# Performance work log

Hardware: AMD Instinct MI355X
Metric: run time of the kernel (lower is better)

Reference implementation:

```python
import jax, jax.numpy as jnp
import numpy as np
import math

B, S, DIM, H, KVH = 2, 2048, 2048, 16, 4
HD = DIM // H          # 128
G = H // KVH           # 4 (GQA repeat factor)
NEG = -1e9             # fp32 additive mask value (matches torch path)


def _rotate_half(x):
    x1, x2 = jnp.split(x, 2, axis=-1)
    return jnp.concatenate([-x2, x1], axis=-1)


def setup_inputs() -> dict:
    key = jax.random.key(0)
    ks = jax.random.split(key, 8)
    hidden_states = jax.random.normal(ks[0], (B, S, DIM), jnp.float32)
    # standard RoPE tables [S, HD]
    inv_freq = 1.0 / (10000.0 ** (jnp.arange(0, HD, 2, dtype=jnp.float32) / HD))
    freqs = jnp.outer(jnp.arange(S, dtype=jnp.float32), inv_freq)
    emb = jnp.concatenate([freqs, freqs], axis=-1)
    position_cos = jnp.cos(emb)
    position_sin = jnp.sin(emb)
    alibi_bias = jax.random.normal(ks[1], (B, S, S), jnp.float32) * 0.01
    attention_mask = jnp.zeros((B, 1, 1, S), jnp.float32)
    sc = 0.02
    wq = jax.random.normal(ks[2], (DIM, DIM), jnp.float32) * sc
    wk = jax.random.normal(ks[3], (DIM, KVH * HD), jnp.float32) * sc
    wv = jax.random.normal(ks[4], (DIM, KVH * HD), jnp.float32) * sc
    wo = jax.random.normal(ks[5], (DIM, DIM), jnp.float32) * sc
    return {"hidden_states": hidden_states, "position_cos": position_cos,
            "position_sin": position_sin, "alibi_bias": alibi_bias,
            "attention_mask": attention_mask, "wq": wq, "wk": wk, "wv": wv, "wo": wo}


def reference(hidden_states, position_cos, position_sin, alibi_bias,
              attention_mask, wq, wk, wv, wo):
    b, s, d = hidden_states.shape
    # projections (weights stored as [in, out])
    q = (hidden_states @ wq).reshape(b, s, H, HD).transpose(0, 2, 1, 3)      # [B,H,S,HD]
    k = (hidden_states @ wk).reshape(b, s, KVH, HD).transpose(0, 2, 1, 3)    # [B,KVH,S,HD]
    v = (hidden_states @ wv).reshape(b, s, KVH, HD).transpose(0, 2, 1, 3)
    # RoPE
    cos = position_cos[None, None]  # [1,1,S,HD]
    sin = position_sin[None, None]
    q = q * cos + _rotate_half(q) * sin
    k = k * cos + _rotate_half(k) * sin
    # GQA repeat kv heads
    k = jnp.repeat(k, G, axis=1)   # [B,H,S,HD]
    v = jnp.repeat(v, G, axis=1)
    scores = jnp.einsum('bhqd,bhkd->bhqk', q, k) * (1.0 / math.sqrt(HD))
    causal = jnp.triu(jnp.full((s, s), NEG, jnp.float32), 1)
    scores = scores + causal + alibi_bias[:, None, :, :] + attention_mask
    attn = jax.nn.softmax(scores.astype(jnp.float32), axis=-1).astype(q.dtype)
    out = jnp.einsum('bhqk,bhkd->bhqd', attn, v)                              # [B,H,S,HD]
    out = out.transpose(0, 2, 1, 3).reshape(b, s, d)
    return out @ wo
```

## Files before the change

kernel.cpp:

```cpp
#include <hip/hip_runtime.h>
#include <hip/hip_bf16.h>

#define Bb   2
#define Ss   2048
#define Dd   2048
#define Hh   16
#define KVHh 4
#define HDd  128
#define QKVW 3072

typedef __bf16 bf16x8 __attribute__((ext_vector_type(8)));
typedef float f32x4 __attribute__((ext_vector_type(4)));

__device__ __forceinline__ unsigned short f2bf(float f) {
    unsigned u = __float_as_uint(f);
    unsigned r = (u + 0x7FFFu + ((u >> 16) & 1u)) >> 16;
    return (unsigned short)r;
}
__device__ __forceinline__ float bfu2f(unsigned short u) {
    return __uint_as_float(((unsigned)u) << 16);
}

#define GLOAD16(g, l) __builtin_amdgcn_global_load_lds( \
    (const __attribute__((address_space(1))) unsigned int*)(g), \
    (__attribute__((address_space(3))) unsigned int*)(l), 16, 0, 0)

__global__ __launch_bounds__(256)
void cast_bf16(const float* __restrict__ X, unsigned short* __restrict__ Y)
{
    int idx = blockIdx.x * 256 + threadIdx.x;
    float4 v = reinterpret_cast<const float4*>(X)[idx];
    ushort4 o;
    o.x = f2bf(v.x); o.y = f2bf(v.y); o.z = f2bf(v.z); o.w = f2bf(v.w);
    reinterpret_cast<ushort4*>(Y)[idx] = o;
}

__global__ __launch_bounds__(256)
void wt_cast_all(const float* __restrict__ wq, const float* __restrict__ wk,
                 const float* __restrict__ wv, const float* __restrict__ wo,
                 unsigned short* __restrict__ wqkvT, unsigned short* __restrict__ woT)
{
    __shared__ float tile[32][33];
    int id = blockIdx.x;
    const float* W; unsigned short* WT; int N, kx, ny;
    if (id < 4096)      {            W = wq; WT = wqkvT;                        N = 2048; kx = id & 63; ny = id >> 6; }
    else if (id < 5120) { id -= 4096; W = wk; WT = wqkvT + (size_t)2048 * 2048; N = 512;  kx = id & 63; ny = id >> 6; }
    else if (id < 6144) { id -= 5120; W = wv; WT = wqkvT + (size_t)2560 * 2048; N = 512;  kx = id & 63; ny = id >> 6; }
    else                { id -= 6144; W = wo; WT = woT;                         N = 2048; kx = id & 63; ny = id >> 6; }
    const int K = 2048;
    int k0 = kx * 32, n0 = ny * 32;
    int tx = threadIdx.x & 31, ty = threadIdx.x >> 5;
    #pragma unroll
    for (int i = 0; i < 32; i += 8)
        tile[ty + i][tx] = W[(size_t)(k0 + ty + i) * N + n0 + tx];
    __syncthreads();
    #pragma unroll
    for (int i = 0; i < 32; i += 8)
        WT[(size_t)(n0 + ty + i) * K + k0 + tx] = f2bf(tile[tx][ty + i]);
}

template<bool BF16OUT>
__global__ __launch_bounds__(512, 2)
void gemm256(const unsigned short* __restrict__ A,
             const unsigned short* __restrict__ BT,
             void* __restrict__ Cv, int M, int N, int K)
{
    __shared__ __align__(16) unsigned short sA[4][256 * 32];
    __shared__ __align__(16) unsigned short sB[4][256 * 32];
    const int tid  = threadIdx.x;
    const int w    = tid >> 6;
    const int lane = tid & 63;
    const int m    = lane & 15;
    const int quad = lane >> 4;
    const int wm   = w >> 2;
    const int wn   = w & 3;
    const int m0   = blockIdx.y * 256, n0 = blockIdx.x * 256;

    const int srow = tid >> 2;
    const int scol = (tid & 3) ^ (((tid >> 5) & 1) << 1);
    const int chk  = quad ^ (((m >> 3) & 1) << 1);

    f32x4 acc[8][4];
    #pragma unroll
    for (int fm = 0; fm < 8; ++fm)
        #pragma unroll
        for (int fn = 0; fn < 4; ++fn) acc[fm][fn] = (f32x4){0.f, 0.f, 0.f, 0.f};

    auto STAGE2 = [&](int T, int h) {
        const int buf = T & 3;
        GLOAD16(A  + (size_t)(m0 + h * 128 + srow) * K + T * 32 + scol * 8,
                (char*)sA + buf * 16384 + h * 8192 + w * 1024);
        GLOAD16(BT + (size_t)(n0 + h * 128 + srow) * K + T * 32 + scol * 8,
                (char*)sB + buf * 16384 + h * 8192 + w * 1024);
    };

    const int NT = K >> 5;

    STAGE2(0, 0); STAGE2(0, 1); STAGE2(1, 0); STAGE2(1, 1);
    asm volatile("s_waitcnt vmcnt(4)" ::: "memory");
    __builtin_amdgcn_s_barrier();
    __builtin_amdgcn_sched_barrier(0);

    #pragma unroll 1
    for (int t = 0; t < NT; ++t) {
        const int buf = t & 3;
        const char* ab = (const char*)sA + buf * 16384 + wm * 8192;
        const char* bb = (const char*)sB + buf * 16384 + (wn >> 1) * 8192 + (wn & 1) * 4096;

        bf16x8 bf[4], af[4];
        #pragma unroll
        for (int fn = 0; fn < 4; ++fn)
            bf[fn] = *(const bf16x8*)(bb + (fn * 16 + m) * 64 + chk * 16);
        #pragma unroll
        for (int j = 0; j < 4; ++j)
            af[j] = *(const bf16x8*)(ab + (j * 16 + m) * 64 + chk * 16);
        if (t + 2 < NT) STAGE2(t + 2, 0);
        __builtin_amdgcn_sched_barrier(0);
        __builtin_amdgcn_s_barrier();
        __builtin_amdgcn_sched_barrier(0);
        __builtin_amdgcn_s_setprio(1);
        #pragma unroll
        for (int j = 0; j < 4; ++j)
            #pragma unroll
            for (int fn = 0; fn < 4; ++fn)
                acc[j][fn] = __builtin_amdgcn_mfma_f32_16x16x32_bf16(
                    af[j], bf[fn], acc[j][fn], 0, 0, 0);
        __builtin_amdgcn_s_setprio(0);
        __builtin_amdgcn_s_barrier();
        __builtin_amdgcn_sched_barrier(0);

        #pragma unroll
        for (int j = 0; j < 4; ++j)
            af[j] = *(const bf16x8*)(ab + ((4 + j) * 16 + m) * 64 + chk * 16);
        if (t + 2 < NT) STAGE2(t + 2, 1);
        __builtin_amdgcn_sched_barrier(0);
        __builtin_amdgcn_s_barrier();
        __builtin_amdgcn_sched_barrier(0);
        __builtin_amdgcn_s_setprio(1);
        #pragma unroll
        for (int j = 0; j < 4; ++j)
            #pragma unroll
            for (int fn = 0; fn < 4; ++fn)
                acc[4 + j][fn] = __builtin_amdgcn_mfma_f32_16x16x32_bf16(
                    af[j], bf[fn], acc[4 + j][fn], 0, 0, 0);
        __builtin_amdgcn_s_setprio(0);

        if (t + 2 < NT)      asm volatile("s_waitcnt vmcnt(4)" ::: "memory");
        else if (t + 1 < NT) asm volatile("s_waitcnt vmcnt(0)" ::: "memory");
        __builtin_amdgcn_s_barrier();
        __builtin_amdgcn_sched_barrier(0);
    }

    #pragma unroll
    for (int fm = 0; fm < 8; ++fm)
        #pragma unroll
        for (int fn = 0; fn < 4; ++fn)
            #pragma unroll
            for (int e = 0; e < 4; ++e) {
                size_t row = m0 + wm * 128 + fm * 16 + quad * 4 + e;
                size_t col = n0 + wn * 64 + fn * 16 + m;
                if (BF16OUT)
                    ((unsigned short*)Cv)[row * N + col] = f2bf(acc[fm][fn][e]);
                else
                    ((float*)Cv)[row * N + col] = acc[fm][fn][e];
            }
}

__global__ __launch_bounds__(256)
void rope_all(unsigned short* __restrict__ qkv, const float* __restrict__ cosT,
              const float* __restrict__ sinT)
{
    const int h   = blockIdx.y;
    const int row = blockIdx.x * 4 + (threadIdx.x >> 6);
    const int i   = threadIdx.x & 63;
    const int s   = row & (Ss - 1);
    const float scale = (h < Hh) ? 0.08838834764831845f : 1.0f;
    unsigned short* xp = qkv + (size_t)row * QKVW + h * HDd;
    float x1 = bfu2f(xp[i]);
    float x2 = bfu2f(xp[i + 64]);
    float c1 = cosT[s * HDd + i];
    float c2 = cosT[s * HDd + i + 64];
    float s1 = sinT[s * HDd + i];
    float s2 = sinT[s * HDd + i + 64];
    xp[i]      = f2bf((x1 * c1 - x2 * s1) * scale);
    xp[i + 64] = f2bf((x2 * c2 + x1 * s2) * scale);
}

__global__ __launch_bounds__(256)
void vt_cast_bf(const unsigned short* __restrict__ KV,
                unsigned short* __restrict__ VT)
{
    __shared__ unsigned short tile[32][34];
    int st = blockIdx.x * 32, dt = blockIdx.y * 32;
    int bk = blockIdx.z;
    int b = bk >> 2, kvh = bk & 3;
    int tx = threadIdx.x & 31, ty = threadIdx.x >> 5;
    #pragma unroll
    for (int i = 0; i < 32; i += 8)
        tile[ty + i][tx] = KV[(size_t)(b * Ss + st + ty + i) * QKVW + 2560 + kvh * HDd + dt + tx];
    __syncthreads();
    #pragma unroll
    for (int i = 0; i < 32; i += 8)
        VT[(((size_t)b * KVHh + kvh) * HDd + dt + ty + i) * Ss + st + tx] =
            tile[tx][ty + i];
}

__global__ __launch_bounds__(256, 2)
void flash_attn(const unsigned short* __restrict__ qkv,
                const unsigned short* __restrict__ VT,
                const float* __restrict__ alibi,
                const float* __restrict__ amask,
                unsigned short* __restrict__ ctx)
{
    __shared__ __align__(16) unsigned short kbuf[3][32 * 128];
    __shared__ __align__(16) unsigned short vbuf[3][128 * 32];
    __shared__ __align__(16) float          abuf[3][2][512];
    __shared__ __align__(16) float          am_lds[Ss];
    __shared__ unsigned short s_p[4][16][56];

    const int tid  = threadIdx.x;
    const int w    = tid >> 6;
    const int m    = tid & 15;
    const int quad = (tid & 63) >> 4;

    const int kvh = blockIdx.y;
    const int b   = blockIdx.z;
    const int h   = kvh * 4 + w;

    const int x    = blockIdx.x;
    const int qtA0 = (x & 1) ? (63 - (x >> 1)) : (x >> 1);
    const int qtA  = b ? (63 - qtA0) : qtA0;
    const int qtB  = 127 - qtA;
    const int qA0  = qtA * 16, qB0 = qtB * 16;
    const int ntA  = (qA0 + 47) >> 5;
    const int ntB  = (qB0 + 47) >> 5;

    const unsigned short* vt0 = VT + ((size_t)b * KVHh + kvh) * HDd * Ss;
    const float* amrow = amask + (size_t)b * Ss;
    const float* arowA = alibi + ((size_t)b * Ss + qA0) * Ss;
    const float* arowB = alibi + ((size_t)b * Ss + qB0) * Ss;
    const unsigned short* kgbase = qkv + (size_t)b * Ss * QKVW + 2048 + kvh * HDd;

    const int krow_s = tid >> 4;
    const int koff_b = ((tid & 15) * 16) ^ ((krow_s & 7) << 4);
    const int vrow_s = tid >> 2;
    const int vchk_s = (tid & 3) ^ ((vrow_s >> 1) & 3);
    const int dstw   = w * 512;

    {
        const float* ag = amrow + tid * 4;
        GLOAD16(ag,        am_lds + w * 256);
        GLOAD16(ag + 1024, am_lds + 1024 + w * 256);
    }
    bf16x8 qaA[4], qaB[4];
    {
        const unsigned short* qrA = qkv + (size_t)(b * Ss + qA0 + m) * QKVW + h * HDd;
        const unsigned short* qrB = qkv + (size_t)(b * Ss + qB0 + m) * QKVW + h * HDd;
        #pragma unroll
        for (int c = 0; c < 4; ++c) {
            qaA[c] = *reinterpret_cast<const bf16x8*>(qrA + c * 32 + quad * 8);
            qaB[c] = *reinterpret_cast<const bf16x8*>(qrB + c * 32 + quad * 8);
        }
    }

    f32x4 oA[8], oB[8];
    #pragma unroll
    for (int f = 0; f < 8; ++f) {
        oA[f] = (f32x4){0.f, 0.f, 0.f, 0.f};
        oB[f] = (f32x4){0.f, 0.f, 0.f, 0.f};
    }
    float lA[4] = {0.f, 0.f, 0.f, 0.f}, lB[4] = {0.f, 0.f, 0.f, 0.f};

    auto STAGE = [&](int kn, int buf, bool aact) {
        const unsigned short* kg =
            kgbase + (size_t)(kn + krow_s) * QKVW + (koff_b >> 1);
        GLOAD16(kg,              &kbuf[buf][dstw]);
        GLOAD16(kg + 16 * QKVW,  &kbuf[buf][2048 + dstw]);
        const unsigned short* vg = vt0 + (size_t)vrow_s * Ss + kn + vchk_s * 8;
        GLOAD16(vg,             &vbuf[buf][dstw]);
        GLOAD16(vg + 64 * Ss,   &vbuf[buf][2048 + dstw]);
        if (tid < 128) {
            if (aact) {
                const float* ag = arowA + (size_t)(tid >> 3) * Ss + kn + (tid & 7) * 4;
                GLOAD16(ag, &abuf[buf][0][w * 256]);
            }
        } else {
            const float* ag = arowB + (size_t)((tid - 128) >> 3) * Ss + kn + (tid & 7) * 4;
            GLOAD16(ag, &abuf[buf][1][(w - 2) * 256]);
        }
    };

    STAGE(0, 0, true);
    asm volatile("s_waitcnt vmcnt(0)" ::: "memory");
    __syncthreads();

    int cur = 0;
    #pragma unroll 1
    for (int kt = 0; kt < ntB; ++kt) {
        const int k0  = kt * 32;
        const int nxt = (cur == 2) ? 0 : cur + 1;
        const bool aact = kt < ntA;

        if (kt + 1 < ntB) {
            const bool aactn = (kt + 1) < ntA;
            STAGE(k0 + 32, nxt, aactn);
            if (w < 2) {
                if (aactn) asm volatile("s_waitcnt vmcnt(5)" ::: "memory");
                else       asm volatile("s_waitcnt vmcnt(4)" ::: "memory");
            } else       asm volatile("s_waitcnt vmcnt(5)" ::: "memory");
        } else {
            asm volatile("s_waitcnt vmcnt(0)" ::: "memory");
        }
        __builtin_amdgcn_s_barrier();
        __builtin_amdgcn_sched_barrier(0);

        const float am0 = am_lds[k0 + m];
        const float am1 = am_lds[k0 + 16 + m];

        const char* kb  = (const char*)&kbuf[cur][0];
        const char* vbp = (const char*)&vbuf[cur][0];
        const int  ksw  = (m & 7) << 4;
        const int  vsw  = ((m >> 1) & 3) << 4;
        bf16x8 kf0[4], kf1[4];
        #pragma unroll
        for (int c = 0; c < 4; ++c) {
            kf0[c] = *(const bf16x8*)(kb + m * 256        + ((c * 64 + quad * 16) ^ ksw));
            kf1[c] = *(const bf16x8*)(kb + (16 + m) * 256 + ((c * 64 + quad * 16) ^ ksw));
        }
        bf16x8 vf[8];
        #pragma unroll
        for (int f = 0; f < 8; ++f)
            vf[f] = *(const bf16x8*)(vbp + (f * 16 + m) * 64 + ((quad * 16) ^ vsw));

        {
            f32x4 s0 = {0.f, 0.f, 0.f, 0.f}, s1 = {0.f, 0.f, 0.f, 0.f};
            #pragma unroll
            for (int c = 0; c < 4; ++c) {
                s0 = __builtin_amdgcn_mfma_f32_16x16x32_bf16(qaB[c], kf0[c], s0, 0, 0, 0);
                s1 = __builtin_amdgcn_mfma_f32_16x16x32_bf16(qaB[c], kf1[c], s1, 0, 0, 0);
            }
            #pragma unroll
            for (int r = 0; r < 4; ++r) {
                const int row = quad * 4 + r;
                const int qi  = qB0 + row;
                float x0 = s0[r] + abuf[cur][1][row * 32 + m]      + am0;
                float x1 = s1[r] + abuf[cur][1][row * 32 + 16 + m] + am1;
                x0 = (k0 + m      <= qi) ? x0 : -1e30f;
                x1 = (k0 + 16 + m <= qi) ? x1 : -1e30f;
                const float p0 = __expf(x0);
                const float p1 = __expf(x1);
                lB[r] += p0 + p1;
                s_p[w][row][m]      = f2bf(p0);
                s_p[w][row][16 + m] = f2bf(p1);
            }
            __builtin_amdgcn_wave_barrier();
            const bf16x8 pa = *reinterpret_cast<const bf16x8*>(&s_p[w][m][quad * 8]);
            __builtin_amdgcn_wave_barrier();
            #pragma unroll
            for (int f = 0; f < 8; ++f)
                oB[f] = __builtin_amdgcn_mfma_f32_16x16x32_bf16(pa, vf[f], oB[f], 0, 0, 0);
        }

        if (aact) {
            f32x4 s0 = {0.f, 0.f, 0.f, 0.f}, s1 = {0.f, 0.f, 0.f, 0.f};
            #pragma unroll
            for (int c = 0; c < 4; ++c) {
                s0 = __builtin_amdgcn_mfma_f32_16x16x32_bf16(qaA[c], kf0[c], s0, 0, 0, 0);
                s1 = __builtin_amdgcn_mfma_f32_16x16x32_bf16(qaA[c], kf1[c], s1, 0, 0, 0);
            }
            #pragma unroll
            for (int r = 0; r < 4; ++r) {
                const int row = quad * 4 + r;
                const int qi  = qA0 + row;
                float x0 = s0[r] + abuf[cur][0][row * 32 + m]      + am0;
                float x1 = s1[r] + abuf[cur][0][row * 32 + 16 + m] + am1;
                x0 = (k0 + m      <= qi) ? x0 : -1e30f;
                x1 = (k0 + 16 + m <= qi) ? x1 : -1e30f;
                const float p0 = __expf(x0);
                const float p1 = __expf(x1);
                lA[r] += p0 + p1;
                s_p[w][row][m]      = f2bf(p0);
                s_p[w][row][16 + m] = f2bf(p1);
            }
            __builtin_amdgcn_wave_barrier();
            const bf16x8 pa = *reinterpret_cast<const bf16x8*>(&s_p[w][m][quad * 8]);
            __builtin_amdgcn_wave_barrier();
            #pragma unroll
            for (int f = 0; f < 8; ++f)
                oA[f] = __builtin_amdgcn_mfma_f32_16x16x32_bf16(pa, vf[f], oA[f], 0, 0, 0);
        }

        cur = nxt;
    }

    float invA[4], invB[4];
    #pragma unroll
    for (int r = 0; r < 4; ++r) {
        float la = lA[r], lb = lB[r];
        la += __shfl_xor(la, 1, 64); lb += __shfl_xor(lb, 1, 64);
        la += __shfl_xor(la, 2, 64); lb += __shfl_xor(lb, 2, 64);
        la += __shfl_xor(la, 4, 64); lb += __shfl_xor(lb, 4, 64);
        la += __shfl_xor(la, 8, 64); lb += __shfl_xor(lb, 8, 64);
        invA[r] = 1.f / la; invB[r] = 1.f / lb;
    }
    #pragma unroll
    for (int f = 0; f < 8; ++f)
        #pragma unroll
        for (int r = 0; r < 4; ++r) {
            ctx[(size_t)(b * Ss + qA0 + quad * 4 + r) * Dd + h * HDd + f * 16 + m] =
                f2bf(oA[f][r] * invA[r]);
            ctx[(size_t)(b * Ss + qB0 + quad * 4 + r) * Dd + h * HDd + f * 16 + m] =
                f2bf(oB[f][r] * invB[r]);
        }
}

extern "C" void kernel_launch(void* const* d_in, const int* in_sizes, int n_in,
                              void* d_out, int out_size, void* d_ws, size_t ws_size,
                              hipStream_t stream) {
    const float* hidden = (const float*)d_in[0];
    const float* cosT   = (const float*)d_in[1];
    const float* sinT   = (const float*)d_in[2];
    const float* alibi  = (const float*)d_in[3];
    const float* amask  = (const float*)d_in[4];
    const float* wq     = (const float*)d_in[5];
    const float* wk     = (const float*)d_in[6];
    const float* wv     = (const float*)d_in[7];
    const float* wo     = (const float*)d_in[8];
    float* out = (float*)d_out;

    char* ws = (char*)d_ws;
    unsigned short* Abf    = (unsigned short*)(ws);
    unsigned short* wqkvT  = (unsigned short*)(ws + 16777216);
    unsigned short* woT    = (unsigned short*)(ws + 29360128);
    unsigned short* QKVraw = (unsigned short*)(ws + 37748736);
    unsigned short* VT     = (unsigned short*)(ws + 62914560);
    unsigned short* Ctx    = (unsigned short*)(ws + 67108864);

    const int M = Bb * Ss;

    cast_bf16<<<(M * Dd / 4) / 256, 256, 0, stream>>>(hidden, Abf);
    wt_cast_all<<<10240, 256, 0, stream>>>(wq, wk, wv, wo, wqkvT, woT);

    gemm256<true><<<dim3(QKVW / 256, M / 256), 512, 0, stream>>>(Abf, wqkvT, QKVraw, M, QKVW, Dd);

    rope_all<<<dim3(M / 4, 20), 256, 0, stream>>>(QKVraw, cosT, sinT);

    vt_cast_bf<<<dim3(Ss / 32, HDd / 32, Bb * KVHh), 256, 0, stream>>>(QKVraw, VT);

    flash_attn<<<dim3(64, KVHh, Bb), 256, 0, stream>>>(QKVraw, VT, alibi, amask, Ctx);

    gemm256<false><<<dim3(Dd / 256, M / 256), 512, 0, stream>>>(Ctx, woT, out, M, Dd, Dd);
}
```

Baseline: 363.6 us.

## Fuse prep kernels, move Q RoPE into attention, shrink GEMM M-tile

```diff
diff --git a/kernel.cpp b/kernel.cpp
--- a/kernel.cpp
+++ b/kernel.cpp
@@ -11,6 +11,7 @@
 
 typedef __bf16 bf16x8 __attribute__((ext_vector_type(8)));
 typedef float f32x4 __attribute__((ext_vector_type(4)));
+typedef unsigned short us8 __attribute__((ext_vector_type(8)));
 
 __device__ __forceinline__ unsigned short f2bf(float f) {
     unsigned u = __float_as_uint(f);
@@ -26,29 +27,30 @@
     (__attribute__((address_space(3))) unsigned int*)(l), 16, 0, 0)
 
 __global__ __launch_bounds__(256)
-void cast_bf16(const float* __restrict__ X, unsigned short* __restrict__ Y)
-{
-    int idx = blockIdx.x * 256 + threadIdx.x;
-    float4 v = reinterpret_cast<const float4*>(X)[idx];
-    ushort4 o;
-    o.x = f2bf(v.x); o.y = f2bf(v.y); o.z = f2bf(v.z); o.w = f2bf(v.w);
-    reinterpret_cast<ushort4*>(Y)[idx] = o;
-}
-
-__global__ __launch_bounds__(256)
-void wt_cast_all(const float* __restrict__ wq, const float* __restrict__ wk,
-                 const float* __restrict__ wv, const float* __restrict__ wo,
-                 unsigned short* __restrict__ wqkvT, unsigned short* __restrict__ woT)
+void prep(const float* __restrict__ hidden,
+          const float* __restrict__ wq, const float* __restrict__ wk,
+          const float* __restrict__ wv, const float* __restrict__ wo,
+          unsigned short* __restrict__ Abf,
+          unsigned short* __restrict__ wqkvT, unsigned short* __restrict__ woT)
 {
     __shared__ float tile[32][33];
     int id = blockIdx.x;
-    const float* W; unsigned short* WT; int N, kx, ny;
-    if (id < 4096)      {            W = wq; WT = wqkvT;                        N = 2048; kx = id & 63; ny = id >> 6; }
-    else if (id < 5120) { id -= 4096; W = wk; WT = wqkvT + (size_t)2048 * 2048; N = 512;  kx = id & 63; ny = id >> 6; }
-    else if (id < 6144) { id -= 5120; W = wv; WT = wqkvT + (size_t)2560 * 2048; N = 512;  kx = id & 63; ny = id >> 6; }
-    else                { id -= 6144; W = wo; WT = woT;                         N = 2048; kx = id & 63; ny = id >> 6; }
+    if (id < 8192) {
+        int idx = id * 256 + threadIdx.x;
+        float4 v = reinterpret_cast<const float4*>(hidden)[idx];
+        ushort4 o;
+        o.x = f2bf(v.x); o.y = f2bf(v.y); o.z = f2bf(v.z); o.w = f2bf(v.w);
+        reinterpret_cast<ushort4*>(Abf)[idx] = o;
+        return;
+    }
+    id -= 8192;
+    const float* W; unsigned short* WT; int N;
+    if (id < 4096)      {            W = wq; WT = wqkvT;                        N = 2048; }
+    else if (id < 5120) { id -= 4096; W = wk; WT = wqkvT + (size_t)2048 * 2048; N = 512;  }
+    else if (id < 6144) { id -= 5120; W = wv; WT = wqkvT + (size_t)2560 * 2048; N = 512;  }
+    else                { id -= 6144; W = wo; WT = woT;                         N = 2048; }
     const int K = 2048;
-    int k0 = kx * 32, n0 = ny * 32;
+    int k0 = (id & 63) * 32, n0 = (id >> 6) * 32;
     int tx = threadIdx.x & 31, ty = threadIdx.x >> 5;
     #pragma unroll
     for (int i = 0; i < 32; i += 8)
@@ -65,7 +67,7 @@
              const unsigned short* __restrict__ BT,
              void* __restrict__ Cv, int M, int N, int K)
 {
-    __shared__ __align__(16) unsigned short sA[4][256 * 32];
+    __shared__ __align__(16) unsigned short sA[4][128 * 32];
     __shared__ __align__(16) unsigned short sB[4][256 * 32];
     const int tid  = threadIdx.x;
     const int w    = tid >> 6;
@@ -74,90 +76,93 @@
     const int quad = lane >> 4;
     const int wm   = w >> 2;
     const int wn   = w & 3;
-    const int m0   = blockIdx.y * 256, n0 = blockIdx.x * 256;
+    const int m0   = blockIdx.y * 128, n0 = blockIdx.x * 256;
 
     const int srow = tid >> 2;
     const int scol = (tid & 3) ^ (((tid >> 5) & 1) << 1);
     const int chk  = quad ^ (((m >> 3) & 1) << 1);
 
-    f32x4 acc[8][4];
-    #pragma unroll
-    for (int fm = 0; fm < 8; ++fm)
+    f32x4 acc[4][4];
+    #pragma unroll
+    for (int fm = 0; fm < 4; ++fm)
         #pragma unroll
         for (int fn = 0; fn < 4; ++fn) acc[fm][fn] = (f32x4){0.f, 0.f, 0.f, 0.f};
 
-    auto STAGE2 = [&](int T, int h) {
-        const int buf = T & 3;
-        GLOAD16(A  + (size_t)(m0 + h * 128 + srow) * K + T * 32 + scol * 8,
-                (char*)sA + buf * 16384 + h * 8192 + w * 1024);
+    auto STAGE_A = [&](int T) {
+        GLOAD16(A + (size_t)(m0 + srow) * K + T * 32 + scol * 8,
+                (char*)sA + (T & 3) * 8192 + w * 1024);
+    };
+    auto STAGE_B = [&](int T, int h) {
         GLOAD16(BT + (size_t)(n0 + h * 128 + srow) * K + T * 32 + scol * 8,
-                (char*)sB + buf * 16384 + h * 8192 + w * 1024);
+                (char*)sB + (T & 3) * 16384 + h * 8192 + w * 1024);
     };
 
     const int NT = K >> 5;
 
-    STAGE2(0, 0); STAGE2(0, 1); STAGE2(1, 0); STAGE2(1, 1);
-    asm volatile("s_waitcnt vmcnt(4)" ::: "memory");
+    STAGE_A(0); STAGE_B(0, 0); STAGE_B(0, 1);
+    STAGE_A(1); STAGE_B(1, 0); STAGE_B(1, 1);
+    asm volatile("s_waitcnt vmcnt(3)" ::: "memory");
     __builtin_amdgcn_s_barrier();
     __builtin_amdgcn_sched_barrier(0);
 
     #pragma unroll 1
     for (int t = 0; t < NT; ++t) {
         const int buf = t & 3;
-        const char* ab = (const char*)sA + buf * 16384 + wm * 8192;
-        const char* bb = (const char*)sB + buf * 16384 + (wn >> 1) * 8192 + (wn & 1) * 4096;
-
-        bf16x8 bf[4], af[4];
+        const char* ab = (const char*)sA + buf * 8192  + wm * 4096;
+        const char* bb = (const char*)sB + buf * 16384 + wn * 4096;
+
+        bf16x8 bf[4], af0[2];
         #pragma unroll
         for (int fn = 0; fn < 4; ++fn)
             bf[fn] = *(const bf16x8*)(bb + (fn * 16 + m) * 64 + chk * 16);
         #pragma unroll
-        for (int j = 0; j < 4; ++j)
-            af[j] = *(const bf16x8*)(ab + (j * 16 + m) * 64 + chk * 16);
-        if (t + 2 < NT) STAGE2(t + 2, 0);
+        for (int j = 0; j < 2; ++j)
+            af0[j] = *(const bf16x8*)(ab + (j * 16 + m) * 64 + chk * 16);
+        if (t + 2 < NT) STAGE_A(t + 2);
         __builtin_amdgcn_sched_barrier(0);
         __builtin_amdgcn_s_barrier();
         __builtin_amdgcn_sched_barrier(0);
         __builtin_amdgcn_s_setprio(1);
         #pragma unroll
-        for (int j = 0; j < 4; ++j)
+        for (int j = 0; j < 2; ++j)
             #pragma unroll
             for (int fn = 0; fn < 4; ++fn)
                 acc[j][fn] = __builtin_amdgcn_mfma_f32_16x16x32_bf16(
-                    af[j], bf[fn], acc[j][fn], 0, 0, 0);
+                    af0[j], bf[fn], acc[j][fn], 0, 0, 0);
         __builtin_amdgcn_s_setprio(0);
         __builtin_amdgcn_s_barrier();
         __builtin_amdgcn_sched_barrier(0);
 
-        #pragma unroll
-        for (int j = 0; j < 4; ++j)
-            af[j] = *(const bf16x8*)(ab + ((4 + j) * 16 + m) * 64 + chk * 16);
-        if (t + 2 < NT) STAGE2(t + 2, 1);
+        bf16x8 af1[2];
+        #pragma unroll
+        for (int j = 0; j < 2; ++j)
+            af1[j] = *(const bf16x8*)(ab + ((2 + j) * 16 + m) * 64 + chk * 16);
+        if (t + 2 < NT) { STAGE_B(t + 2, 0); STAGE_B(t + 2, 1); }
         __builtin_amdgcn_sched_barrier(0);
         __builtin_amdgcn_s_barrier();
         __builtin_amdgcn_sched_barrier(0);
         __builtin_amdgcn_s_setprio(1);
         #pragma unroll
-        for (int j = 0; j < 4; ++j)
+        for (int j = 0; j < 2; ++j)
             #pragma unroll
             for (int fn = 0; fn < 4; ++fn)
-                acc[4 + j][fn] = __builtin_amdgcn_mfma_f32_16x16x32_bf16(
-                    af[j], bf[fn], acc[4 + j][fn], 0, 0, 0);
+                acc[2 + j][fn] = __builtin_amdgcn_mfma_f32_16x16x32_bf16(
+                    af1[j], bf[fn], acc[2 + j][fn], 0, 0, 0);
         __builtin_amdgcn_s_setprio(0);
 
-        if (t + 2 < NT)      asm volatile("s_waitcnt vmcnt(4)" ::: "memory");
+        if (t + 2 < NT)      asm volatile("s_waitcnt vmcnt(3)" ::: "memory");
         else if (t + 1 < NT) asm volatile("s_waitcnt vmcnt(0)" ::: "memory");
         __builtin_amdgcn_s_barrier();
         __builtin_amdgcn_sched_barrier(0);
     }
 
     #pragma unroll
-    for (int fm = 0; fm < 8; ++fm)
+    for (int fm = 0; fm < 4; ++fm)
         #pragma unroll
         for (int fn = 0; fn < 4; ++fn)
             #pragma unroll
             for (int e = 0; e < 4; ++e) {
-                size_t row = m0 + wm * 128 + fm * 16 + quad * 4 + e;
+                size_t row = m0 + wm * 64 + fm * 16 + quad * 4 + e;
                 size_t col = n0 + wn * 64 + fn * 16 + m;
                 if (BF16OUT)
                     ((unsigned short*)Cv)[row * N + col] = f2bf(acc[fm][fn][e]);
@@ -167,41 +172,39 @@
 }
 
 __global__ __launch_bounds__(256)
-void rope_all(unsigned short* __restrict__ qkv, const float* __restrict__ cosT,
-              const float* __restrict__ sinT)
-{
-    const int h   = blockIdx.y;
-    const int row = blockIdx.x * 4 + (threadIdx.x >> 6);
-    const int i   = threadIdx.x & 63;
-    const int s   = row & (Ss - 1);
-    const float scale = (h < Hh) ? 0.08838834764831845f : 1.0f;
-    unsigned short* xp = qkv + (size_t)row * QKVW + h * HDd;
-    float x1 = bfu2f(xp[i]);
-    float x2 = bfu2f(xp[i + 64]);
-    float c1 = cosT[s * HDd + i];
-    float c2 = cosT[s * HDd + i + 64];
-    float s1 = sinT[s * HDd + i];
-    float s2 = sinT[s * HDd + i + 64];
-    xp[i]      = f2bf((x1 * c1 - x2 * s1) * scale);
-    xp[i + 64] = f2bf((x2 * c2 + x1 * s2) * scale);
-}
-
-__global__ __launch_bounds__(256)
-void vt_cast_bf(const unsigned short* __restrict__ KV,
-                unsigned short* __restrict__ VT)
+void kv_prep(unsigned short* __restrict__ qkv, const float* __restrict__ cosT,
+             const float* __restrict__ sinT, unsigned short* __restrict__ VT)
 {
     __shared__ unsigned short tile[32][34];
-    int st = blockIdx.x * 32, dt = blockIdx.y * 32;
-    int bk = blockIdx.z;
-    int b = bk >> 2, kvh = bk & 3;
+    int id = blockIdx.x;
+    if (id < 4096) {
+        const int h   = 16 + (id & 3);
+        const int row = (id >> 2) * 4 + (threadIdx.x >> 6);
+        const int i   = threadIdx.x & 63;
+        const int s   = row & (Ss - 1);
+        unsigned short* xp = qkv + (size_t)row * QKVW + h * HDd;
+        float x1 = bfu2f(xp[i]);
+        float x2 = bfu2f(xp[i + 64]);
+        float c1 = cosT[s * HDd + i], c2 = cosT[s * HDd + i + 64];
+        float s1 = sinT[s * HDd + i], s2 = sinT[s * HDd + i + 64];
+        xp[i]      = f2bf(x1 * c1 - x2 * s1);
+        xp[i + 64] = f2bf(x2 * c2 + x1 * s2);
+        return;
+    }
+    id -= 4096;
+    int st = (id & 63) * 32;
+    int dt = ((id >> 6) & 3) * 32;
+    int bk = id >> 8;
+    int bq = bk >> 2, kvh = bk & 3;
     int tx = threadIdx.x & 31, ty = threadIdx.x >> 5;
     #pragma unroll
     for (int i = 0; i < 32; i += 8)
-        tile[ty + i][tx] = KV[(size_t)(b * Ss + st + ty + i) * QKVW + 2560 + kvh * HDd + dt + tx];
+        tile[ty + i][tx] =
+            qkv[(size_t)(bq * Ss + st + ty + i) * QKVW + 2560 + kvh * HDd + dt + tx];
     __syncthreads();
     #pragma unroll
     for (int i = 0; i < 32; i += 8)
-        VT[(((size_t)b * KVHh + kvh) * HDd + dt + ty + i) * Ss + st + tx] =
+        VT[(((size_t)bq * KVHh + kvh) * HDd + dt + ty + i) * Ss + st + tx] =
             tile[tx][ty + i];
 }
 
@@ -210,6 +213,8 @@
                 const unsigned short* __restrict__ VT,
                 const float* __restrict__ alibi,
                 const float* __restrict__ amask,
+                const float* __restrict__ cosT,
+                const float* __restrict__ sinT,
                 unsigned short* __restrict__ ctx)
 {
     __shared__ __align__(16) unsigned short kbuf[3][32 * 128];
@@ -252,16 +257,47 @@
         GLOAD16(ag,        am_lds + w * 256);
         GLOAD16(ag + 1024, am_lds + 1024 + w * 256);
     }
+
     bf16x8 qaA[4], qaB[4];
-    {
-        const unsigned short* qrA = qkv + (size_t)(b * Ss + qA0 + m) * QKVW + h * HDd;
-        const unsigned short* qrB = qkv + (size_t)(b * Ss + qB0 + m) * QKVW + h * HDd;
+    auto LOADQ = [&](int q0v, bf16x8 (&qa)[4]) {
+        const unsigned short* qrow = qkv + (size_t)(b * Ss + q0v + m) * QKVW + h * HDd;
+        const float* cb = cosT + (size_t)(q0v + m) * HDd + quad * 8;
+        const float* sb = sinT + (size_t)(q0v + m) * HDd + quad * 8;
+        float xv[4][8], cs[4][8], sn[4][8];
         #pragma unroll
         for (int c = 0; c < 4; ++c) {
-            qaA[c] = *reinterpret_cast<const bf16x8*>(qrA + c * 32 + quad * 8);
-            qaB[c] = *reinterpret_cast<const bf16x8*>(qrB + c * 32 + quad * 8);
-        }
-    }
+            us8 uq = *reinterpret_cast<const us8*>(qrow + c * 32 + quad * 8);
+            float4 c0 = *reinterpret_cast<const float4*>(cb + c * 32);
+            float4 c1 = *reinterpret_cast<const float4*>(cb + c * 32 + 4);
+            float4 s0 = *reinterpret_cast<const float4*>(sb + c * 32);
+            float4 s1 = *reinterpret_cast<const float4*>(sb + c * 32 + 4);
+            #pragma unroll
+            for (int e = 0; e < 8; ++e) xv[c][e] = bfu2f(uq[e]);
+            cs[c][0] = c0.x; cs[c][1] = c0.y; cs[c][2] = c0.z; cs[c][3] = c0.w;
+            cs[c][4] = c1.x; cs[c][5] = c1.y; cs[c][6] = c1.z; cs[c][7] = c1.w;
+            sn[c][0] = s0.x; sn[c][1] = s0.y; sn[c][2] = s0.z; sn[c][3] = s0.w;
+            sn[c][4] = s1.x; sn[c][5] = s1.y; sn[c][6] = s1.z; sn[c][7] = s1.w;
+        }
+        const float qsc = 0.08838834764831845f;
+        #pragma unroll
+        for (int c = 0; c < 2; ++c)
+            #pragma unroll
+            for (int e = 0; e < 8; ++e) {
+                float lo = xv[c][e] * cs[c][e]         - xv[c + 2][e] * sn[c][e];
+                float hi = xv[c + 2][e] * cs[c + 2][e] + xv[c][e]     * sn[c + 2][e];
+                xv[c][e]     = lo * qsc;
+                xv[c + 2][e] = hi * qsc;
+            }
+        #pragma unroll
+        for (int c = 0; c < 4; ++c) {
+            us8 o;
+            #pragma unroll
+            for (int e = 0; e < 8; ++e) o[e] = f2bf(xv[c][e]);
+            qa[c] = __builtin_bit_cast(bf16x8, o);
+        }
+    };
+    LOADQ(qA0, qaA);
+    LOADQ(qB0, qaB);
 
     f32x4 oA[8], oB[8];
     #pragma unroll
@@ -438,16 +474,13 @@
 
     const int M = Bb * Ss;
 
-    cast_bf16<<<(M * Dd / 4) / 256, 256, 0, stream>>>(hidden, Abf);
-    wt_cast_all<<<10240, 256, 0, stream>>>(wq, wk, wv, wo, wqkvT, woT);
-
-    gemm256<true><<<dim3(QKVW / 256, M / 256), 512, 0, stream>>>(Abf, wqkvT, QKVraw, M, QKVW, Dd);
-
-    rope_all<<<dim3(M / 4, 20), 256, 0, stream>>>(QKVraw, cosT, sinT);
-
-    vt_cast_bf<<<dim3(Ss / 32, HDd / 32, Bb * KVHh), 256, 0, stream>>>(QKVraw, VT);
-
-    flash_attn<<<dim3(64, KVHh, Bb), 256, 0, stream>>>(QKVraw, VT, alibi, amask, Ctx);
-
-    gemm256<false><<<dim3(Dd / 256, M / 256), 512, 0, stream>>>(Ctx, woT, out, M, Dd, Dd);
-}
+    prep<<<8192 + 10240, 256, 0, stream>>>(hidden, wq, wk, wv, wo, Abf, wqkvT, woT);
+
+    gemm256<true><<<dim3(QKVW / 256, M / 128), 512, 0, stream>>>(Abf, wqkvT, QKVraw, M, QKVW, Dd);
+
+    kv_prep<<<4096 + 2048, 256, 0, stream>>>(QKVraw, cosT, sinT, VT);
+
+    flash_attn<<<dim3(64, KVHh, Bb), 256, 0, stream>>>(QKVraw, VT, alibi, amask, cosT, sinT, Ctx);
+
+    gemm256<false><<<dim3(Dd / 256, M / 128), 512, 0, stream>>>(Ctx, woT, out, M, Dd, Dd);
+}
```

Result: slower. 388.6 us (+6.9%).
